# Performance work log

Measured on AMD Instinct MI355X. Metric: run time of the kernel, lower is better.

## Reference

```python
import jax, jax.numpy as jnp
import numpy as np

NUM_BINS = 11  # len of each cut vector
ITERATIONS = 20
INPUT_DIM = 16777216


def _transform_cut(c):
    # torch: sort(.data), clamp(0,1), pin endpoints to 0 and 1 (done on .data -> no grad)
    s = jnp.clip(jnp.sort(c), 0.0, 1.0)
    s = s.at[0].set(0.0).at[-1].set(1.0)
    return jax.lax.stop_gradient(s)


def setup_inputs() -> dict:
    key = jax.random.key(0)
    kx, kr, kg, kb = jax.random.split(key, 4)
    # pixel values in [0, 255) to match the *255 cut scaling in the module
    x = jax.random.uniform(kx, (INPUT_DIM, 4), dtype=jnp.float32) * 255.0
    r_cut = jax.random.uniform(kr, (11,), dtype=jnp.float32)
    g_cut = jax.random.uniform(kg, (11,), dtype=jnp.float32)
    b_cut = jax.random.uniform(kb, (11,), dtype=jnp.float32)
    return {"x": x, "r_cut": r_cut, "g_cut": g_cut, "b_cut": b_cut}


def reference(x, r_cut, g_cut, b_cut):
    n = NUM_BINS
    rc = _transform_cut(r_cut)
    gc = _transform_cut(g_cut)
    bc = _transform_cut(b_cut)

    # per-pixel searchsorted binning (torch.searchsorted, right=False == side='left')
    r_iv = jnp.searchsorted(rc * 255.0, x[:, 0])
    g_iv = jnp.searchsorted(gc * 255.0, x[:, 1])
    b_iv = jnp.searchsorted(bc * 255.0, x[:, 2])

    # counts[r-1, g-1, b-1] += 1 ; torch negative indexing (r-1 == -1) wraps -> mod n
    flat_idx = ((r_iv - 1) % n) * (n * n) + ((g_iv - 1) % n) * n + ((b_iv - 1) % n)
    counts = jnp.bincount(flat_idx, length=n * n * n).astype(jnp.float32)

    # top 2*iterations bins (descending count)
    order = jnp.argsort(-counts)
    top = order[: 2 * ITERATIONS]
    top_r = (top // (n * n)) % n
    top_g = (top // n) % n
    top_b = top % n
    # flat index -> (r,g,b) is bijective, so all triples are unique: dedup == take first ITERATIONS
    tr = top_r[:ITERATIONS]
    tg = top_g[:ITERATIONS]
    tb = top_b[:ITERATIONS]

    # output values: clamp((val-1), 0, n-2), then bin-center-ish reconstruction
    r = jnp.clip(tr, 0, n - 2)
    g = jnp.clip(tg, 0, n - 2)
    b = jnp.clip(tb, 0, n - 2)
    r_val = 255.0 * r / n + (rc[r + 1] - rc[r]) * 255.0 / 2.0
    g_val = 255.0 * g / n + (gc[g + 1] - gc[g]) * 255.0 / 2.0
    b_val = 255.0 * b / n + (bc[b + 1] - bc[b]) * 255.0 / 2.0
    a_val = jnp.full((ITERATIONS,), 255.0, dtype=jnp.float32)
    return jnp.stack([r_val, g_val, b_val, a_val], axis=1)  # [iterations, 4]
```

## Files before the change

kernel.cpp:

```cpp
#include <hip/hip_runtime.h>

#define NBINS 1331
#define NCUT  11
#define TOPK  20

#define WS_HIST_OFF   0
#define WS_CUT255_OFF 8192
#define WS_CUTRAW_OFF (8192 + 33 * 4)

__global__ void prep_kernel(const float* __restrict__ r_cut,
                            const float* __restrict__ g_cut,
                            const float* __restrict__ b_cut,
                            float* __restrict__ cut255,
                            float* __restrict__ cutraw) {
    int t = threadIdx.x;
    if (t < 3) {
        const float* src = (t == 0) ? r_cut : ((t == 1) ? g_cut : b_cut);
        float s[NCUT];
        for (int i = 0; i < NCUT; ++i) s[i] = src[i];
        for (int i = 1; i < NCUT; ++i) {
            float v = s[i];
            int j = i - 1;
            while (j >= 0 && s[j] > v) { s[j + 1] = s[j]; --j; }
            s[j + 1] = v;
        }
        for (int i = 0; i < NCUT; ++i) s[i] = fminf(fmaxf(s[i], 0.0f), 1.0f);
        s[0] = 0.0f;
        s[NCUT - 1] = 1.0f;
        for (int i = 0; i < NCUT; ++i) {
            cutraw[t * NCUT + i] = s[i];
            cut255[t * NCUT + i] = s[i] * 255.0f;
        }
    }
}

__global__ __launch_bounds__(256) void hist_kernel(const float4* __restrict__ x,
                                                   const float* __restrict__ cut255,
                                                   unsigned int* __restrict__ ghist,
                                                   int npix) {
    __shared__ unsigned int sh[NBINS];
    for (int i = threadIdx.x; i < NBINS; i += blockDim.x) sh[i] = 0;

    float cr[NCUT], cg[NCUT], cb[NCUT];
#pragma unroll
    for (int j = 0; j < NCUT; ++j) {
        cr[j] = cut255[j];
        cg[j] = cut255[NCUT + j];
        cb[j] = cut255[2 * NCUT + j];
    }
    __syncthreads();

    int stride = gridDim.x * blockDim.x;
    for (int i = blockIdx.x * blockDim.x + threadIdx.x; i < npix; i += stride) {
        float4 v = x[i];
        int r = 0, g = 0, b = 0;
#pragma unroll
        for (int j = 0; j < NCUT; ++j) {
            r += (cr[j] < v.x);
            g += (cg[j] < v.y);
            b += (cb[j] < v.z);
        }
        r = r ? (r - 1) : (NCUT - 1);
        g = g ? (g - 1) : (NCUT - 1);
        b = b ? (b - 1) : (NCUT - 1);
        atomicAdd(&sh[r * 121 + g * 11 + b], 1u);
    }
    __syncthreads();
    for (int i = threadIdx.x; i < NBINS; i += blockDim.x) {
        unsigned int c = sh[i];
        if (c) atomicAdd(&ghist[i], c);
    }
}

__global__ __launch_bounds__(256) void topk_kernel(const unsigned int* __restrict__ ghist,
                                                   const float* __restrict__ cutraw,
                                                   float* __restrict__ out) {
    __shared__ unsigned long long key[NBINS];
    __shared__ unsigned long long red[256];
    __shared__ int topbin[TOPK];
    int t = threadIdx.x;

    for (int i = t; i < NBINS; i += 256)
        key[i] = ((unsigned long long)ghist[i] << 11) |
                 (unsigned long long)(2047 - i);
    __syncthreads();

    for (int it = 0; it < TOPK; ++it) {
        unsigned long long m = 0ull;
        for (int i = t; i < NBINS; i += 256) {
            unsigned long long k = key[i];
            m = (k > m) ? k : m;
        }
        red[t] = m;
        __syncthreads();
        for (int s = 128; s > 0; s >>= 1) {
            if (t < s) {
                unsigned long long a = red[t], b2 = red[t + s];
                red[t] = (b2 > a) ? b2 : a;
            }
            __syncthreads();
        }
        if (t == 0) {
            int bin = 2047 - (int)(red[0] & 2047ull);
            topbin[it] = bin;
            key[bin] = 0ull;
        }
        __syncthreads();
    }

    if (t < TOPK) {
        int bin = topbin[t];
        int tr = (bin / 121) % NCUT;
        int tg = (bin / 11) % NCUT;
        int tb = bin % NCUT;
        int r = min(tr, NCUT - 2);
        int g = min(tg, NCUT - 2);
        int b = min(tb, NCUT - 2);
        const float* rc = cutraw;
        const float* gc = cutraw + NCUT;
        const float* bc = cutraw + 2 * NCUT;
        float4 o;
        o.x = 255.0f * (float)r / 11.0f + (rc[r + 1] - rc[r]) * 255.0f / 2.0f;
        o.y = 255.0f * (float)g / 11.0f + (gc[g + 1] - gc[g]) * 255.0f / 2.0f;
        o.z = 255.0f * (float)b / 11.0f + (bc[b + 1] - bc[b]) * 255.0f / 2.0f;
        o.w = 255.0f;
        reinterpret_cast<float4*>(out)[t] = o;
    }
}

extern "C" void kernel_launch(void* const* d_in, const int* in_sizes, int n_in,
                              void* d_out, int out_size, void* d_ws, size_t ws_size,
                              hipStream_t stream) {
    const float* x     = (const float*)d_in[0];
    const float* r_cut = (const float*)d_in[1];
    const float* g_cut = (const float*)d_in[2];
    const float* b_cut = (const float*)d_in[3];
    float* out = (float*)d_out;

    int npix = in_sizes[0] / 4;

    unsigned int* ghist = (unsigned int*)((char*)d_ws + WS_HIST_OFF);
    float* cut255       = (float*)((char*)d_ws + WS_CUT255_OFF);
    float* cutraw       = (float*)((char*)d_ws + WS_CUTRAW_OFF);

    hipMemsetAsync(ghist, 0, NBINS * sizeof(unsigned int), stream);

    prep_kernel<<<1, 64, 0, stream>>>(r_cut, g_cut, b_cut, cut255, cutraw);

    hist_kernel<<<1024, 256, 0, stream>>>((const float4*)x, cut255, ghist, npix);

    topk_kernel<<<1, 256, 0, stream>>>(ghist, cutraw, out);
}
```

Before: 391.4 us.

## Fuse cut prep into hist/topk kernels, unroll pixel loop, wave-level top-k

The separate prep kernel is removed. Each histogram block now sorts the cut vectors into shared memory, and the top-k kernel recomputes the raw cuts itself. The histogram loop handles two pixels per iteration to get more loads in flight. The top-k step now runs as a single 64-lane wave that holds keys in registers and reduces with shuffles instead of shared-memory tree reductions with barriers. In exchange, every hist block repeats the small sort, and the top-k kernel carries more registers per thread.

```diff
diff --git a/kernel.cpp b/kernel.cpp
--- a/kernel.cpp
+++ b/kernel.cpp
@@ -3,113 +3,131 @@
 #define NBINS 1331
 #define NCUT  11
 #define TOPK  20
+#define HIST_BLOCKS 1024
+#define HIST_THREADS 256
 
 #define WS_HIST_OFF   0
-#define WS_CUT255_OFF 8192
-#define WS_CUTRAW_OFF (8192 + 33 * 4)
 
-__global__ void prep_kernel(const float* __restrict__ r_cut,
-                            const float* __restrict__ g_cut,
-                            const float* __restrict__ b_cut,
-                            float* __restrict__ cut255,
-                            float* __restrict__ cutraw) {
+__device__ inline void transform_cut(const float* __restrict__ src, float* dst) {
+    float s[NCUT];
+    for (int i = 0; i < NCUT; ++i) s[i] = src[i];
+    for (int i = 1; i < NCUT; ++i) {
+        float v = s[i];
+        int j = i - 1;
+        while (j >= 0 && s[j] > v) { s[j + 1] = s[j]; --j; }
+        s[j + 1] = v;
+    }
+    for (int i = 0; i < NCUT; ++i) s[i] = fminf(fmaxf(s[i], 0.0f), 1.0f);
+    s[0] = 0.0f;
+    s[NCUT - 1] = 1.0f;
+    for (int i = 0; i < NCUT; ++i) dst[i] = s[i];
+}
+
+__global__ __launch_bounds__(HIST_THREADS) void hist_kernel(
+        const float4* __restrict__ x,
+        const float* __restrict__ r_cut,
+        const float* __restrict__ g_cut,
+        const float* __restrict__ b_cut,
+        unsigned int* __restrict__ ghist,
+        int npix) {
+    __shared__ unsigned int sh[NBINS];
+    __shared__ float scut[3 * NCUT];
+
     int t = threadIdx.x;
+    for (int i = t; i < NBINS; i += HIST_THREADS) sh[i] = 0;
     if (t < 3) {
         const float* src = (t == 0) ? r_cut : ((t == 1) ? g_cut : b_cut);
         float s[NCUT];
-        for (int i = 0; i < NCUT; ++i) s[i] = src[i];
-        for (int i = 1; i < NCUT; ++i) {
-            float v = s[i];
-            int j = i - 1;
-            while (j >= 0 && s[j] > v) { s[j + 1] = s[j]; --j; }
-            s[j + 1] = v;
-        }
-        for (int i = 0; i < NCUT; ++i) s[i] = fminf(fmaxf(s[i], 0.0f), 1.0f);
-        s[0] = 0.0f;
-        s[NCUT - 1] = 1.0f;
-        for (int i = 0; i < NCUT; ++i) {
-            cutraw[t * NCUT + i] = s[i];
-            cut255[t * NCUT + i] = s[i] * 255.0f;
-        }
+        transform_cut(src, s);
+        for (int i = 0; i < NCUT; ++i)
+            scut[t * NCUT + i] = s[i] * 255.0f;
     }
-}
-
-__global__ __launch_bounds__(256) void hist_kernel(const float4* __restrict__ x,
-                                                   const float* __restrict__ cut255,
-                                                   unsigned int* __restrict__ ghist,
-                                                   int npix) {
-    __shared__ unsigned int sh[NBINS];
-    for (int i = threadIdx.x; i < NBINS; i += blockDim.x) sh[i] = 0;
+    __syncthreads();
 
     float cr[NCUT], cg[NCUT], cb[NCUT];
 #pragma unroll
     for (int j = 0; j < NCUT; ++j) {
-        cr[j] = cut255[j];
-        cg[j] = cut255[NCUT + j];
-        cb[j] = cut255[2 * NCUT + j];
+        cr[j] = scut[j];
+        cg[j] = scut[NCUT + j];
+        cb[j] = scut[2 * NCUT + j];
+    }
+
+    const int stride = gridDim.x * HIST_THREADS;
+    int i = blockIdx.x * HIST_THREADS + t;
+    for (; i < npix; i += 2 * stride) {
+        float4 a = x[i];
+        bool has2 = (i + stride) < npix;
+        float4 b = has2 ? x[i + stride] : a;
+
+        int r0 = 0, g0 = 0, b0 = 0, r1 = 0, g1 = 0, b1 = 0;
+#pragma unroll
+        for (int j = 0; j < NCUT; ++j) {
+            r0 += (cr[j] < a.x); g0 += (cg[j] < a.y); b0 += (cb[j] < a.z);
+            r1 += (cr[j] < b.x); g1 += (cg[j] < b.y); b1 += (cb[j] < b.z);
+        }
+        r0 = r0 ? (r0 - 1) : (NCUT - 1);
+        g0 = g0 ? (g0 - 1) : (NCUT - 1);
+        b0 = b0 ? (b0 - 1) : (NCUT - 1);
+        atomicAdd(&sh[r0 * 121 + g0 * 11 + b0], 1u);
+        if (has2) {
+            r1 = r1 ? (r1 - 1) : (NCUT - 1);
+            g1 = g1 ? (g1 - 1) : (NCUT - 1);
+            b1 = b1 ? (b1 - 1) : (NCUT - 1);
+            atomicAdd(&sh[r1 * 121 + g1 * 11 + b1], 1u);
+        }
+    }
+    __syncthreads();
+    for (int j = t; j < NBINS; j += HIST_THREADS) {
+        unsigned int c = sh[j];
+        if (c) atomicAdd(&ghist[j], c);
+    }
+}
+
+#define SLOTS 21
+__global__ __launch_bounds__(64) void topk_kernel(
+        const unsigned int* __restrict__ ghist,
+        const float* __restrict__ r_cut,
+        const float* __restrict__ g_cut,
+        const float* __restrict__ b_cut,
+        float* __restrict__ out) {
+    __shared__ float cutraw[3 * NCUT];
+    int t = threadIdx.x;
+    if (t < 3) {
+        const float* src = (t == 0) ? r_cut : ((t == 1) ? g_cut : b_cut);
+        transform_cut(src, &cutraw[t * NCUT]);
     }
     __syncthreads();
 
-    int stride = gridDim.x * blockDim.x;
-    for (int i = blockIdx.x * blockDim.x + threadIdx.x; i < npix; i += stride) {
-        float4 v = x[i];
-        int r = 0, g = 0, b = 0;
+    unsigned long long k[SLOTS];
 #pragma unroll
-        for (int j = 0; j < NCUT; ++j) {
-            r += (cr[j] < v.x);
-            g += (cg[j] < v.y);
-            b += (cb[j] < v.z);
-        }
-        r = r ? (r - 1) : (NCUT - 1);
-        g = g ? (g - 1) : (NCUT - 1);
-        b = b ? (b - 1) : (NCUT - 1);
-        atomicAdd(&sh[r * 121 + g * 11 + b], 1u);
+    for (int s = 0; s < SLOTS; ++s) {
+        int bin = t + 64 * s;
+        k[s] = (bin < NBINS)
+                 ? (((unsigned long long)ghist[bin] << 11) |
+                    (unsigned long long)(2047 - bin))
+                 : 0ull;
     }
-    __syncthreads();
-    for (int i = threadIdx.x; i < NBINS; i += blockDim.x) {
-        unsigned int c = sh[i];
-        if (c) atomicAdd(&ghist[i], c);
-    }
-}
 
-__global__ __launch_bounds__(256) void topk_kernel(const unsigned int* __restrict__ ghist,
-                                                   const float* __restrict__ cutraw,
-                                                   float* __restrict__ out) {
-    __shared__ unsigned long long key[NBINS];
-    __shared__ unsigned long long red[256];
-    __shared__ int topbin[TOPK];
-    int t = threadIdx.x;
-
-    for (int i = t; i < NBINS; i += 256)
-        key[i] = ((unsigned long long)ghist[i] << 11) |
-                 (unsigned long long)(2047 - i);
-    __syncthreads();
-
+    int mybin = 0;
+#pragma unroll 1
     for (int it = 0; it < TOPK; ++it) {
         unsigned long long m = 0ull;
-        for (int i = t; i < NBINS; i += 256) {
-            unsigned long long k = key[i];
-            m = (k > m) ? k : m;
+#pragma unroll
+        for (int s = 0; s < SLOTS; ++s) m = (k[s] > m) ? k[s] : m;
+#pragma unroll
+        for (int d = 1; d < 64; d <<= 1) {
+            unsigned long long o = __shfl_xor(m, d);
+            m = (o > m) ? o : m;
         }
-        red[t] = m;
-        __syncthreads();
-        for (int s = 128; s > 0; s >>= 1) {
-            if (t < s) {
-                unsigned long long a = red[t], b2 = red[t + s];
-                red[t] = (b2 > a) ? b2 : a;
-            }
-            __syncthreads();
-        }
-        if (t == 0) {
-            int bin = 2047 - (int)(red[0] & 2047ull);
-            topbin[it] = bin;
-            key[bin] = 0ull;
-        }
-        __syncthreads();
+        int bin = 2047 - (int)(m & 2047ull);
+        if (it == t) mybin = bin;
+#pragma unroll
+        for (int s = 0; s < SLOTS; ++s)
+            if (bin == t + 64 * s) k[s] = 0ull;
     }
 
     if (t < TOPK) {
-        int bin = topbin[t];
+        int bin = mybin;
         int tr = (bin / 121) % NCUT;
         int tg = (bin / 11) % NCUT;
         int tb = bin % NCUT;
@@ -140,14 +158,11 @@
     int npix = in_sizes[0] / 4;
 
     unsigned int* ghist = (unsigned int*)((char*)d_ws + WS_HIST_OFF);
-    float* cut255       = (float*)((char*)d_ws + WS_CUT255_OFF);
-    float* cutraw       = (float*)((char*)d_ws + WS_CUTRAW_OFF);
 
     hipMemsetAsync(ghist, 0, NBINS * sizeof(unsigned int), stream);
 
-    prep_kernel<<<1, 64, 0, stream>>>(r_cut, g_cut, b_cut, cut255, cutraw);
+    hist_kernel<<<HIST_BLOCKS, HIST_THREADS, 0, stream>>>(
+        (const float4*)x, r_cut, g_cut, b_cut, ghist, npix);
 
-    hist_kernel<<<1024, 256, 0, stream>>>((const float4*)x, cut255, ghist, npix);
-
-    topk_kernel<<<1, 256, 0, stream>>>(ghist, cutraw, out);
+    topk_kernel<<<1, 64, 0, stream>>>(ghist, r_cut, g_cut, b_cut, out);
 }
```

Result: slower. 405.1 us (+3.5%).
